# Performance work log

Measured on AMD Instinct MI355X. Metric: run time of the kernel, lower is better.

Reference implementation:

```python
import jax, jax.numpy as jnp
import numpy as np

N_HEADS_ROUTER = 8
N_HEADS_INPUT = 4
LN_EPS = 1e-5

def gelu(x):
    return jax.nn.gelu(x, approximate=False)  # torch F.gelu default (erf)

def mha(x, wq, wk, wv, bq, bk, bv, wo, bo, n_heads):
    # PyTorch nn.MultiheadAttention (batch_first, eval mode)
    B, S, E = x.shape
    d = E // n_heads
    scale = 1.0 / np.sqrt(d).astype(np.float32)
    def split(t):
        return t.reshape(B, S, n_heads, d).transpose(0, 2, 1, 3)  # [B,H,S,d]
    q = split(x @ wq.T + bq)
    k = split(x @ wk.T + bk)
    v = split(x @ wv.T + bv)
    attn = jax.nn.softmax(jnp.einsum('bhqd,bhkd->bhqk', q, k) * scale, axis=-1)
    o = jnp.einsum('bhqk,bhkd->bhqd', attn, v).transpose(0, 2, 1, 3).reshape(B, S, E)
    return o @ wo.T + bo

def layer_norm(x, g, b):
    mu = x.mean(axis=-1, keepdims=True)
    var = ((x - mu) ** 2).mean(axis=-1, keepdims=True)
    return (x - mu) * jax.lax.rsqrt(var + LN_EPS) * g + b

def setup_inputs() -> dict:
    key = jax.random.key(0)
    ks = jax.random.split(key, 20)
    B, S, D, NI, NP = 4, 1024, 1024, 512, 1024
    def rn(k, shape, s=0.02):
        return jax.random.normal(k, shape, jnp.float32) * s
    return {
        'x': jax.random.normal(ks[0], (B, S, D), jnp.float32),
        # DynamicRouter MHA (embed=d_model, 8 heads)
        'r_wq': rn(ks[1], (D, D)), 'r_wk': rn(ks[2], (D, D)), 'r_wv': rn(ks[3], (D, D)),
        'r_bq': jnp.zeros((D,), jnp.float32), 'r_bk': jnp.zeros((D,), jnp.float32), 'r_bv': jnp.zeros((D,), jnp.float32),
        'r_wo': rn(ks[4], (D, D)), 'r_bo': jnp.zeros((D,), jnp.float32),
        'aff_w': rn(ks[5], (NI, D)), 'aff_b': jnp.zeros((NI,), jnp.float32),
        # InputNeurons
        'patterns': rn(ks[6], (NI, D), 0.05),
        'i_wq': rn(ks[7], (NI, NI)), 'i_wk': rn(ks[8], (NI, NI)), 'i_wv': rn(ks[9], (NI, NI)),
        'i_bq': jnp.zeros((NI,), jnp.float32), 'i_bk': jnp.zeros((NI,), jnp.float32), 'i_bv': jnp.zeros((NI,), jnp.float32),
        'i_wo': rn(ks[10], (NI, NI)), 'i_bo': jnp.zeros((NI,), jnp.float32),
        'ln_g': jnp.ones((NI,), jnp.float32), 'ln_b': jnp.zeros((NI,), jnp.float32),
        # ProcessNeurons
        'comb_w': rn(ks[11], (NP, NI), 0.05),
        'proj_w': rn(ks[12], (NP, D), 0.05),
        'k_input': 256,
        'k_process': 512,
    }

def reference(x, r_wq, r_wk, r_wv, r_bq, r_bk, r_bv, r_wo, r_bo, aff_w, aff_b,
              patterns, i_wq, i_wk, i_wv, i_bq, i_bk, i_bv, i_wo, i_bo,
              ln_g, ln_b, comb_w, proj_w, k_input, k_process):
    B, S, D = x.shape
    NI = aff_w.shape[0]
    # --- DynamicRouter ---
    context = mha(x, r_wq, r_wk, r_wv, r_bq, r_bk, r_bv, r_wo, r_bo, N_HEADS_ROUTER)
    affinity = context @ aff_w.T + aff_b           # [B,S,NI]
    scores = affinity.max(axis=1)                  # [B,NI] (max-pool over seq)
    probs = jax.nn.softmax(scores, axis=-1)
    _, idx = jax.lax.top_k(scores, k_input)        # [B,k_in]
    one_hot = jax.nn.one_hot(idx, NI, dtype=probs.dtype).sum(axis=1)  # [B,NI]
    weights = jax.lax.stop_gradient(one_hot - probs) + probs          # straight-through
    # --- InputNeurons ---
    act = gelu(context @ patterns.T)               # [B,S,NI]
    attn_out = mha(act, i_wq, i_wk, i_wv, i_bq, i_bk, i_bv, i_wo, i_bo, N_HEADS_INPUT)
    act = layer_norm(act + attn_out, ln_g, ln_b)
    # --- select input neurons ---
    weighted = act * weights[:, None, :]
    sel = jnp.take_along_axis(weighted, jnp.broadcast_to(idx[:, None, :], (B, S, k_input)), axis=2)  # [B,S,k_in]
    # --- ProcessNeurons ---
    sel_w = comb_w[:, idx].transpose(1, 0, 2)      # [B, NP, k_in]
    pa = gelu(jnp.einsum('bsk,bpk->bsp', sel, sel_w))  # [B,S,NP]
    ps = pa.mean(axis=1)                            # [B,NP]
    _, pidx = jax.lax.top_k(ps, k_process)          # [B,k_p]
    spa = jnp.take_along_axis(pa, jnp.broadcast_to(pidx[:, None, :], (B, S, k_process)), axis=2)  # [B,S,k_p]
    sproj = proj_w[pidx]                            # [B,k_p,D]
    return jnp.einsum('bsk,bkd->bsd', spa, sproj)   # [B,S,D]
```

## Files before the change

### kernel.cpp

```cpp
#include <hip/hip_runtime.h>
#include <math.h>

#define DEVI static __device__ __forceinline__

typedef __attribute__((ext_vector_type(8))) short short8;
typedef __attribute__((ext_vector_type(4))) float f32x4;
typedef unsigned short u16;

DEVI float gelu_f(float x) {
    return 0.5f * x * (1.0f + erff(x * 0.7071067811865475f));
}
DEVI u16 f2bf(float f) {
    unsigned u = __builtin_bit_cast(unsigned, f);
    return (u16)((u + 0x7fffu + ((u >> 16) & 1u)) >> 16);
}
DEVI float bf2f(u16 b) {
    unsigned u = ((unsigned)b) << 16;
    return __builtin_bit_cast(float, u);
}
DEVI void split_bf(float v, u16& h, u16& l) {
    h = f2bf(v);
    l = f2bf(v - bf2f(h));
}

template<int BN, bool SPLIT, bool DO_GELU, int OMODE>
__global__ __launch_bounds__(256, 2)
void gemm_planes(const u16* __restrict__ Agh, const u16* __restrict__ Agl,
                 const u16* __restrict__ Bgh, const u16* __restrict__ Bgl,
                 const float* __restrict__ bias, float* __restrict__ Cf,
                 u16* __restrict__ O1h, u16* __restrict__ O1l,
                 u16* __restrict__ O2h, u16* __restrict__ O2l,
                 u16* __restrict__ O3h, u16* __restrict__ O3l,
                 int M, int N, int K, int HH, int partN)
{
    constexpr int BM = 128, BK = 64, PK = 72;
    constexpr int NPL = SPLIT ? 2 : 1;
    constexpr int MF  = (BN == 128) ? 4 : 2;
    __shared__ __align__(16) u16 As[NPL][BM * PK];
    __shared__ __align__(16) u16 Bs[NPL][BN * PK];
    const int t = threadIdx.x, w = t >> 6, l = t & 63;
    const int lr = l & 15, lg = l >> 4;
    const int m0 = blockIdx.y * BM, n0 = blockIdx.x * BN;
    const int moff = (BN == 128) ? (w >> 1) * 64 : w * 32;
    const int noff = (BN == 128) ? (w & 1) * 64 : 0;
    const int srow = t >> 3, sslot = t & 7;

    f32x4 acc[MF][4];
    #pragma unroll
    for (int i = 0; i < MF; ++i)
        #pragma unroll
        for (int j = 0; j < 4; ++j) acc[i][j] = 0.0f;

    for (int k0 = 0; k0 < K; k0 += BK) {
        __syncthreads();
        #pragma unroll
        for (int p = 0; p < 4; ++p) {
            int row = p * 32 + srow;
            size_t g = (size_t)(m0 + row) * K + k0 + sslot * 8;
            *(uint4*)&As[0][row * PK + sslot * 8] = *(const uint4*)&Agh[g];
            if constexpr (SPLIT)
                *(uint4*)&As[1][row * PK + sslot * 8] = *(const uint4*)&Agl[g];
        }
        #pragma unroll
        for (int p = 0; p < BN / 32; ++p) {
            int row = p * 32 + srow;
            size_t g = (size_t)(n0 + row) * K + k0 + sslot * 8;
            *(uint4*)&Bs[0][row * PK + sslot * 8] = *(const uint4*)&Bgh[g];
            if constexpr (SPLIT)
                *(uint4*)&Bs[1][row * PK + sslot * 8] = *(const uint4*)&Bgl[g];
        }
        __syncthreads();
        #pragma unroll
        for (int ks = 0; ks < 2; ++ks) {
            short8 af[MF][NPL], bfr[4][NPL];
            #pragma unroll
            for (int mf = 0; mf < MF; ++mf) {
                int a = (moff + mf * 16 + lr) * PK + ks * 32 + lg * 8;
                af[mf][0] = *(const short8*)&As[0][a];
                if constexpr (SPLIT) af[mf][1] = *(const short8*)&As[1][a];
            }
            #pragma unroll
            for (int nf = 0; nf < 4; ++nf) {
                int a = (noff + nf * 16 + lr) * PK + ks * 32 + lg * 8;
                bfr[nf][0] = *(const short8*)&Bs[0][a];
                if constexpr (SPLIT) bfr[nf][1] = *(const short8*)&Bs[1][a];
            }
            #pragma unroll
            for (int mf = 0; mf < MF; ++mf)
                #pragma unroll
                for (int nf = 0; nf < 4; ++nf) {
                    acc[mf][nf] = __builtin_amdgcn_mfma_f32_16x16x32_bf16(
                        af[mf][0], bfr[nf][0], acc[mf][nf], 0, 0, 0);
                    if constexpr (SPLIT) {
                        acc[mf][nf] = __builtin_amdgcn_mfma_f32_16x16x32_bf16(
                            af[mf][0], bfr[nf][1], acc[mf][nf], 0, 0, 0);
                        acc[mf][nf] = __builtin_amdgcn_mfma_f32_16x16x32_bf16(
                            af[mf][1], bfr[nf][0], acc[mf][nf], 0, 0, 0);
                    }
                }
        }
    }
    #pragma unroll
    for (int mf = 0; mf < MF; ++mf)
        #pragma unroll
        for (int nf = 0; nf < 4; ++nf) {
            int col  = n0 + noff + nf * 16 + lr;
            int mrow = m0 + moff + mf * 16 + lg * 4;
            float bv = bias ? bias[col] : 0.0f;
            float ov[4];
            #pragma unroll
            for (int r = 0; r < 4; ++r) ov[r] = acc[mf][nf][r] + bv;
            if constexpr (OMODE == 0) {
                #pragma unroll
                for (int r = 0; r < 4; ++r) {
                    float o = ov[r];
                    if constexpr (DO_GELU) o = gelu_f(o);
                    Cf[(size_t)(mrow + r) * N + col] = o;
                }
            } else if constexpr (OMODE == 1) {
                #pragma unroll
                for (int r = 0; r < 4; ++r) {
                    float o = ov[r];
                    if constexpr (DO_GELU) o = gelu_f(o);
                    u16 hb, lb; split_bf(o, hb, lb);
                    O1h[(size_t)(mrow + r) * N + col] = hb;
                    O1l[(size_t)(mrow + r) * N + col] = lb;
                }
            } else if constexpr (OMODE == 3) {
                if (col < partN) {
                    #pragma unroll
                    for (int r = 0; r < 4; ++r) {
                        u16 hb, lb; split_bf(ov[r], hb, lb);
                        O1h[(size_t)(mrow + r) * partN + col] = hb;
                        O1l[(size_t)(mrow + r) * partN + col] = lb;
                    }
                } else if (col < 2 * partN) {
                    int c2 = col - partN;
                    #pragma unroll
                    for (int r = 0; r < 4; ++r) {
                        u16 hb, lb; split_bf(ov[r], hb, lb);
                        O2h[(size_t)(mrow + r) * partN + c2] = hb;
                        O2l[(size_t)(mrow + r) * partN + c2] = lb;
                    }
                } else {
                    int c2 = col - 2 * partN;
                    int hh = c2 >> 7, dd = c2 & 127;
                    int bb = mrow >> 10, s0 = mrow & 1023;
                    size_t idx = ((size_t)(bb * HH + hh) * 128 + dd) * 1024 + s0;
                    ushort4 oh, ol;
                    #pragma unroll
                    for (int r = 0; r < 4; ++r) {
                        u16 hb, lb; split_bf(ov[r], hb, lb);
                        ((u16*)&oh)[r] = hb; ((u16*)&ol)[r] = lb;
                    }
                    *(ushort4*)&O3h[idx] = oh;
                    *(ushort4*)&O3l[idx] = ol;
                }
            } else if constexpr (OMODE == 4) {
                if (col < partN) {
                    #pragma unroll
                    for (int r = 0; r < 4; ++r)
                        Cf[(size_t)(mrow + r) * partN + col] = ov[r];
                } else {
                    int c2 = col - partN;
                    #pragma unroll
                    for (int r = 0; r < 4; ++r) {
                        float o = gelu_f(ov[r]);
                        u16 hb, lb; split_bf(o, hb, lb);
                        O1h[(size_t)(mrow + r) * partN + c2] = hb;
                        O1l[(size_t)(mrow + r) * partN + c2] = lb;
                    }
                }
            }
        }
}

__global__ __launch_bounds__(256, 3)
void attn_planes(const u16* __restrict__ Qh, const u16* __restrict__ Ql,
                 const u16* __restrict__ Kh, const u16* __restrict__ Kl,
                 const u16* __restrict__ Vh, const u16* __restrict__ Vl,
                 u16* __restrict__ Oh, u16* __restrict__ Ol,
                 int S, int Dm, int H, float scale)
{
    __shared__ __align__(16) u16 KsL[2][32 * 136];
    __shared__ __align__(16) u16 VsL[2][128 * 40];
    __shared__ __align__(16) u16 PsL[2][4 * 16 * 40];
    const int t = threadIdx.x, w = t >> 6, l = t & 63;
    const int lr = l & 15, lg = l >> 4;
    const int nqt = gridDim.x;
    const int nwg = nqt * gridDim.y;
    const int fid = blockIdx.y * nqt + blockIdx.x;
    const int nid = (fid & 7) * (nwg >> 3) + (fid >> 3);
    const int bh = nid / nqt, qt = nid - bh * nqt;
    const int b = bh / H, h = bh - b * H;
    const int q0 = qt * 64 + w * 16;
    const size_t qkbase = (size_t)(b * S) * Dm + h * 128;
    const size_t vbase  = (size_t)(b * H + h) * 128 * 1024;

    short8 qhf[4], qlf[4];
    #pragma unroll
    for (int ks = 0; ks < 4; ++ks) {
        size_t g = qkbase + (size_t)(q0 + lr) * Dm + ks * 32 + lg * 8;
        qhf[ks] = *(const short8*)&Qh[g];
        qlf[ks] = *(const short8*)&Ql[g];
    }
    f32x4 accO[8];
    #pragma unroll
    for (int i = 0; i < 8; ++i) accO[i] = 0.0f;
    float ls = 0.0f;
    const int pw = w * 640;

    for (int c0 = 0; c0 < S; c0 += 32) {
        __syncthreads();
        #pragma unroll
        for (int p = 0; p < 2; ++p) {
            int key = p * 16 + (t >> 4);
            int slot = t & 15;
            size_t g = qkbase + (size_t)(c0 + key) * Dm + slot * 8;
            *(uint4*)&KsL[0][key * 136 + slot * 8] = *(const uint4*)&Kh[g];
            *(uint4*)&KsL[1][key * 136 + slot * 8] = *(const uint4*)&Kl[g];
        }
        #pragma unroll
        for (int p = 0; p < 2; ++p) {
            int d = p * 64 + (t >> 2);
            int ksl = t & 3;
            size_t g = vbase + (size_t)d * 1024 + c0 + ksl * 8;
            *(uint4*)&VsL[0][d * 40 + ksl * 8] = *(const uint4*)&Vh[g];
            *(uint4*)&VsL[1][d * 40 + ksl * 8] = *(const uint4*)&Vl[g];
        }
        __syncthreads();
        f32x4 sac[2];
        sac[0] = 0.0f; sac[1] = 0.0f;
        #pragma unroll
        for (int mt = 0; mt < 2; ++mt)
            #pragma unroll
            for (int ks = 0; ks < 4; ++ks) {
                int a = (mt * 16 + lr) * 136 + ks * 32 + lg * 8;
                short8 khf = *(const short8*)&KsL[0][a];
                short8 klf = *(const short8*)&KsL[1][a];
                sac[mt] = __builtin_amdgcn_mfma_f32_16x16x32_bf16(khf, qhf[ks], sac[mt], 0, 0, 0);
                sac[mt] = __builtin_amdgcn_mfma_f32_16x16x32_bf16(khf, qlf[ks], sac[mt], 0, 0, 0);
                sac[mt] = __builtin_amdgcn_mfma_f32_16x16x32_bf16(klf, qhf[ks], sac[mt], 0, 0, 0);
            }
        #pragma unroll
        for (int mt = 0; mt < 2; ++mt)
            #pragma unroll
            for (int rr = 0; rr < 4; ++rr) {
                float p = __expf(sac[mt][rr] * scale);
                ls += p;
                int key = mt * 16 + lg * 4 + rr;
                u16 hb, lb; split_bf(p, hb, lb);
                PsL[0][pw + lr * 40 + key] = hb;
                PsL[1][pw + lr * 40 + key] = lb;
            }
        short8 pah = *(const short8*)&PsL[0][pw + lr * 40 + lg * 8];
        short8 pal = *(const short8*)&PsL[1][pw + lr * 40 + lg * 8];
        #pragma unroll
        for (int nt = 0; nt < 8; ++nt) {
            int a = (nt * 16 + lr) * 40 + lg * 8;
            short8 vhf = *(const short8*)&VsL[0][a];
            short8 vlf = *(const short8*)&VsL[1][a];
            accO[nt] = __builtin_amdgcn_mfma_f32_16x16x32_bf16(pah, vhf, accO[nt], 0, 0, 0);
            accO[nt] = __builtin_amdgcn_mfma_f32_16x16x32_bf16(pah, vlf, accO[nt], 0, 0, 0);
            accO[nt] = __builtin_amdgcn_mfma_f32_16x16x32_bf16(pal, vhf, accO[nt], 0, 0, 0);
        }
    }
    float lt = ls + __shfl_xor(ls, 16, 64);
    lt += __shfl_xor(lt, 32, 64);
    #pragma unroll
    for (int rr = 0; rr < 4; ++rr) {
        float inv = 1.0f / __shfl(lt, lg * 4 + rr, 64);
        size_t rowoff = qkbase + (size_t)(q0 + lg * 4 + rr) * Dm;
        #pragma unroll
        for (int nt = 0; nt < 8; ++nt) {
            float o = accO[nt][rr] * inv;
            u16 hb, lb; split_bf(o, hb, lb);
            Oh[rowoff + nt * 16 + lr] = hb;
            Ol[rowoff + nt * 16 + lr] = lb;
        }
    }
}

__global__ __launch_bounds__(256)
void pack_f32(const float* __restrict__ src, u16* __restrict__ dh,
              u16* __restrict__ dl, int n4)
{
    int i = blockIdx.x * 256 + threadIdx.x;
    if (i >= n4) return;
    float4 v = *(const float4*)&src[i * 4];
    ushort4 hv, lv;
    split_bf(v.x, hv.x, lv.x);
    split_bf(v.y, hv.y, lv.y);
    split_bf(v.z, hv.z, lv.z);
    split_bf(v.w, hv.w, lv.w);
    *(ushort4*)&dh[i * 4] = hv;
    *(ushort4*)&dl[i * 4] = lv;
}

__global__ __launch_bounds__(256)
void packT64(const float* __restrict__ src, u16* __restrict__ dh,
             u16* __restrict__ dl, int R, int C)
{
    __shared__ float tile[64][65];
    int r0 = blockIdx.y * 64, c0 = blockIdx.x * 64;
    int t = threadIdx.x;
    #pragma unroll
    for (int i = 0; i < 16; ++i) {
        int idx = i * 256 + t, rr = idx >> 6, cc = idx & 63;
        tile[rr][cc] = src[(size_t)(r0 + rr) * C + c0 + cc];
    }
    __syncthreads();
    #pragma unroll
    for (int i = 0; i < 16; ++i) {
        int idx = i * 256 + t, rr = idx >> 6, cc = idx & 63;
        float v = tile[cc][rr];
        u16 hb, lb; split_bf(v, hb, lb);
        size_t o = (size_t)(c0 + rr) * R + r0 + cc;
        dh[o] = hb; dl[o] = lb;
    }
}

__global__ __launch_bounds__(256)
void mask_rows(u16* __restrict__ ph, const float* __restrict__ mask)
{
    int i = blockIdx.x * 256 + threadIdx.x;
    int i4 = i * 4;
    int bb = i4 >> 20;
    int col = i4 & 1023;
    ushort4 v = *(ushort4*)&ph[i4];
    float4 m = *(const float4*)&mask[bb * 1024 + col];
    if (m.x == 0.f) v.x = 0;
    if (m.y == 0.f) v.y = 0;
    if (m.z == 0.f) v.z = 0;
    if (m.w == 0.f) v.w = 0;
    *(ushort4*)&ph[i4] = v;
}

__global__ __launch_bounds__(256)
void reduce_max_f32(const float* __restrict__ X, float* __restrict__ P, int S, int N)
{
    int n = blockIdx.x * 256 + threadIdx.x;
    int sc = blockIdx.y, bb = blockIdx.z;
    const float* base = X + ((size_t)bb * S + sc * 64) * N + n;
    float acc = -3.402823466e38f;
    for (int s = 0; s < 64; ++s) acc = fmaxf(acc, base[(size_t)s * N]);
    P[((size_t)bb * 16 + sc) * N + n] = acc;
}

__global__ __launch_bounds__(256)
void reduce_sum_planes(const u16* __restrict__ Xh, const u16* __restrict__ Xl,
                       float* __restrict__ P, int S, int N)
{
    int n = blockIdx.x * 256 + threadIdx.x;
    int sc = blockIdx.y, bb = blockIdx.z;
    size_t base = ((size_t)bb * S + sc * 64) * N + n;
    float acc = 0.f;
    for (int s = 0; s < 64; ++s)
        acc += bf2f(Xh[base + (size_t)s * N]) + bf2f(Xl[base + (size_t)s * N]);
    P[((size_t)bb * 16 + sc) * N + n] = acc;
}

template<int OP>
__global__ __launch_bounds__(256)
void reduce_stage2(const float* __restrict__ P, float* __restrict__ Y, int N, float scl)
{
    int n = blockIdx.x * 256 + threadIdx.x;
    int bb = blockIdx.y;
    float acc = (OP == 0) ? -3.402823466e38f : 0.f;
    for (int s = 0; s < 16; ++s) {
        float v = P[((size_t)bb * 16 + s) * N + n];
        acc = (OP == 0) ? fmaxf(acc, v) : (acc + v);
    }
    Y[(size_t)bb * N + n] = (OP == 0) ? acc : acc * scl;
}

template<int N, int KSEL>
__global__ __launch_bounds__(1024)
void topk_mask_kernel(const float* __restrict__ Sc, float* __restrict__ mask)
{
    __shared__ float v[N];
    __shared__ int   id[N];
    int t = threadIdx.x;
    int b = blockIdx.x;
    v[t]  = Sc[b * N + t];
    id[t] = t;
    __syncthreads();
    for (int k = 2; k <= N; k <<= 1) {
        for (int j = k >> 1; j > 0; j >>= 1) {
            int ixj = t ^ j;
            if (ixj > t) {
                bool dir = ((t & k) == 0);
                float va = v[t], vb = v[ixj];
                int   ia = id[t], ib = id[ixj];
                bool before_b = (vb > va) || (vb == va && ib < ia);
                bool sw = dir ? before_b : !before_b;
                if (sw) { v[t] = vb; v[ixj] = va; id[t] = ib; id[ixj] = ia; }
            }
            __syncthreads();
        }
    }
    mask[b * N + id[t]] = (t < KSEL) ? 1.0f : 0.0f;
}

__global__ __launch_bounds__(256)
void ln_mask_planes(const u16* __restrict__ Xh, const u16* __restrict__ Xl,
                    const u16* __restrict__ Rh, const u16* __restrict__ Rl,
                    const float* __restrict__ gam, const float* __restrict__ bet,
                    const float* __restrict__ mask,
                    u16* __restrict__ Yh, u16* __restrict__ Yl)
{
    int row = blockIdx.x, bb = row >> 10, t = threadIdx.x;
    size_t base = (size_t)row * 512;
    float a1 = bf2f(Xh[base + t]) + bf2f(Xl[base + t])
             + bf2f(Rh[base + t]) + bf2f(Rl[base + t]);
    float a2 = bf2f(Xh[base + t + 256]) + bf2f(Xl[base + t + 256])
             + bf2f(Rh[base + t + 256]) + bf2f(Rl[base + t + 256]);
    float s  = a1 + a2;
    float sq = a1 * a1 + a2 * a2;
    #pragma unroll
    for (int off = 32; off > 0; off >>= 1) {
        s  += __shfl_down(s, off, 64);
        sq += __shfl_down(sq, off, 64);
    }
    __shared__ float red[8];
    int wid = t >> 6, lane = t & 63;
    if (lane == 0) { red[wid] = s; red[wid + 4] = sq; }
    __syncthreads();
    if (t == 0) {
        float st  = red[0] + red[1] + red[2] + red[3];
        float sqt = red[4] + red[5] + red[6] + red[7];
        float mu  = st / 512.0f;
        float var = sqt / 512.0f - mu * mu;
        red[0] = mu;
        red[1] = rsqrtf(var + 1e-5f);
    }
    __syncthreads();
    float mu = red[0], rstd = red[1];
    float y1 = ((a1 - mu) * rstd * gam[t] + bet[t]) * mask[bb * 512 + t];
    float y2 = ((a2 - mu) * rstd * gam[t + 256] + bet[t + 256]) * mask[bb * 512 + t + 256];
    u16 hb, lb;
    split_bf(y1, hb, lb); Yh[base + t] = hb;       Yl[base + t] = lb;
    split_bf(y2, hb, lb); Yh[base + t + 256] = hb; Yl[base + t + 256] = lb;
}

extern "C" void kernel_launch(void* const* d_in, const int* in_sizes, int n_in,
                              void* d_out, int out_size, void* d_ws, size_t ws_size,
                              hipStream_t stream)
{
    (void)in_sizes; (void)n_in; (void)out_size; (void)ws_size;
    const float* x        = (const float*)d_in[0];
    const float* r_wq     = (const float*)d_in[1];
    const float* r_wk     = (const float*)d_in[2];
    const float* r_wv     = (const float*)d_in[3];
    const float* r_bq     = (const float*)d_in[4];
    const float* r_bk     = (const float*)d_in[5];
    const float* r_bv     = (const float*)d_in[6];
    const float* r_wo     = (const float*)d_in[7];
    const float* r_bo     = (const float*)d_in[8];
    const float* aff_w    = (const float*)d_in[9];
    const float* aff_b    = (const float*)d_in[10];
    const float* patterns = (const float*)d_in[11];
    const float* i_wq     = (const float*)d_in[12];
    const float* i_wk     = (const float*)d_in[13];
    const float* i_wv     = (const float*)d_in[14];
    const float* i_bq     = (const float*)d_in[15];
    const float* i_bk     = (const float*)d_in[16];
    const float* i_bv     = (const float*)d_in[17];
    const float* i_wo     = (const float*)d_in[18];
    const float* i_bo     = (const float*)d_in[19];
    const float* ln_g     = (const float*)d_in[20];
    const float* ln_b     = (const float*)d_in[21];
    const float* comb_w   = (const float*)d_in[22];
    const float* proj_w   = (const float*)d_in[23];

    constexpr size_t MBy = 1024 * 1024;
    char* base = (char*)d_ws;

    u16* xh   = (u16*)(base);             u16* xl   = (u16*)(base + 8 * MBy);
    u16* aph  = xh;                        u16* apl  = xl;
    float* aff = (float*)base;
    u16* acth = (u16*)(base + 8 * MBy);   u16* actl = (u16*)(base + 12 * MBy);
    u16* rqh  = (u16*)(base + 16 * MBy);  u16* rql  = (u16*)(base + 24 * MBy);
    u16* ctxh = rqh;                       u16* ctxl = rql;
    u16* pah  = rqh;                       u16* pal  = rql;
    u16* rkh  = (u16*)(base + 32 * MBy);  u16* rkl  = (u16*)(base + 40 * MBy);
    u16* iqh  = (u16*)(base + 32 * MBy);  u16* iql  = (u16*)(base + 36 * MBy);
    u16* ikh  = (u16*)(base + 40 * MBy);  u16* ikl  = (u16*)(base + 44 * MBy);
    u16* a2fh = iqh;                       u16* a2fl = iql;
    u16* lnmh = ikh;                       u16* lnml = ikl;
    u16* rvth = (u16*)(base + 48 * MBy);  u16* rvtl = (u16*)(base + 56 * MBy);
    u16* ivth = (u16*)(base + 48 * MBy);  u16* ivtl = (u16*)(base + 52 * MBy);
    u16* a2ph = (u16*)(base + 56 * MBy);  u16* a2pl = (u16*)(base + 60 * MBy);
    u16* wqkvh = (u16*)(base + 64 * MBy); u16* wqkvl = (u16*)(base + 70 * MBy);
    u16* woh   = (u16*)(base + 64 * MBy); u16* wol   = (u16*)(base + 66 * MBy);
    u16* apbh  = (u16*)(base + 68 * MBy); u16* apbl  = (u16*)(base + 70 * MBy);
    u16* iwqkvh = (u16*)(base + 64 * MBy); u16* iwqkvl = (u16*)(base + 66 * MBy);
    u16* iwoh  = (u16*)(base + 68 * MBy); u16* iwol  = (u16*)(base + 69 * MBy);
    u16* cbh   = (u16*)(base + 70 * MBy); u16* cbl   = (u16*)(base + 71 * MBy);
    u16* pjh   = (u16*)(base + 72 * MBy); u16* pjl   = (u16*)(base + 74 * MBy);
    float* partial = (float*)(base + 76 * MBy);
    float* scores  = (float*)(base + 76 * MBy + 262144);
    float* maskI   = scores + 2048;
    float* ps      = maskI + 2048;
    float* maskP   = ps + 4096;
    float* rbias   = maskP + 4096;
    float* ibias   = rbias + 3072;
    float* apbias  = ibias + 1536;

    const float scale = 0.08838834764831843f;
    dim3 blk(256);

    pack_f32<<<4096, blk, 0, stream>>>(x, xh, xl, 1048576);
    pack_f32<<<1024, blk, 0, stream>>>(r_wq, wqkvh, wqkvl, 262144);
    pack_f32<<<1024, blk, 0, stream>>>(r_wk, wqkvh + 1048576, wqkvl + 1048576, 262144);
    pack_f32<<<1024, blk, 0, stream>>>(r_wv, wqkvh + 2097152, wqkvl + 2097152, 262144);
    hipMemcpyAsync(rbias,        r_bq, 4096, hipMemcpyDeviceToDevice, stream);
    hipMemcpyAsync(rbias + 1024, r_bk, 4096, hipMemcpyDeviceToDevice, stream);
    hipMemcpyAsync(rbias + 2048, r_bv, 4096, hipMemcpyDeviceToDevice, stream);

    gemm_planes<128, true, false, 3><<<dim3(24, 32), blk, 0, stream>>>(
        xh, xl, wqkvh, wqkvl, rbias, nullptr,
        rqh, rql, rkh, rkl, rvth, rvtl, 4096, 3072, 1024, 8, 1024);

    pack_f32<<<1024, blk, 0, stream>>>(r_wo, woh, wol, 262144);
    pack_f32<<<512, blk, 0, stream>>>(aff_w, apbh, apbl, 131072);
    pack_f32<<<512, blk, 0, stream>>>(patterns, apbh + 524288, apbl + 524288, 131072);
    hipMemcpyAsync(apbias, aff_b, 2048, hipMemcpyDeviceToDevice, stream);
    hipMemsetAsync(apbias + 512, 0, 2048, stream);

    attn_planes<<<dim3(16, 32), blk, 0, stream>>>(rqh, rql, rkh, rkl, rvth, rvtl,
                                                  aph, apl, 1024, 1024, 8, scale);
    gemm_planes<128, true, false, 1><<<dim3(8, 32), blk, 0, stream>>>(
        aph, apl, woh, wol, r_bo, nullptr,
        ctxh, ctxl, nullptr, nullptr, nullptr, nullptr, 4096, 1024, 1024, 0, 0);

    gemm_planes<128, true, false, 4><<<dim3(8, 32), blk, 0, stream>>>(
        ctxh, ctxl, apbh, apbl, apbias, aff,
        acth, actl, nullptr, nullptr, nullptr, nullptr, 4096, 1024, 1024, 0, 512);
    reduce_max_f32<<<dim3(2, 16, 4), blk, 0, stream>>>(aff, partial, 1024, 512);
    reduce_stage2<0><<<dim3(2, 4), blk, 0, stream>>>(partial, scores, 512, 1.0f);
    topk_mask_kernel<512, 256><<<dim3(4), dim3(512), 0, stream>>>(scores, maskI);

    pack_f32<<<256, blk, 0, stream>>>(i_wq, iwqkvh, iwqkvl, 65536);
    pack_f32<<<256, blk, 0, stream>>>(i_wk, iwqkvh + 262144, iwqkvl + 262144, 65536);
    pack_f32<<<256, blk, 0, stream>>>(i_wv, iwqkvh + 524288, iwqkvl + 524288, 65536);
    pack_f32<<<256, blk, 0, stream>>>(i_wo, iwoh, iwol, 65536);
    pack_f32<<<512, blk, 0, stream>>>(comb_w, cbh, cbl, 131072);
    packT64<<<dim3(16, 16), blk, 0, stream>>>(proj_w, pjh, pjl, 1024, 1024);
    hipMemcpyAsync(ibias,        i_bq, 2048, hipMemcpyDeviceToDevice, stream);
    hipMemcpyAsync(ibias + 512,  i_bk, 2048, hipMemcpyDeviceToDevice, stream);
    hipMemcpyAsync(ibias + 1024, i_bv, 2048, hipMemcpyDeviceToDevice, stream);

    gemm_planes<128, true, false, 3><<<dim3(12, 32), blk, 0, stream>>>(
        acth, actl, iwqkvh, iwqkvl, ibias, nullptr,
        iqh, iql, ikh, ikl, ivth, ivtl, 4096, 1536, 512, 4, 512);
    attn_planes<<<dim3(16, 16), blk, 0, stream>>>(iqh, iql, ikh, ikl, ivth, ivtl,
                                                  a2ph, a2pl, 1024, 512, 4, scale);
    gemm_planes<64, true, false, 1><<<dim3(8, 32), blk, 0, stream>>>(
        a2ph, a2pl, iwoh, iwol, i_bo, nullptr,
        a2fh, a2fl, nullptr, nullptr, nullptr, nullptr, 4096, 512, 512, 0, 0);
    ln_mask_planes<<<dim3(4096), blk, 0, stream>>>(acth, actl, a2fh, a2fl,
                                                   ln_g, ln_b, maskI, lnmh, lnml);

    gemm_planes<128, true, true, 1><<<dim3(8, 32), blk, 0, stream>>>(
        lnmh, lnml, cbh, cbl, nullptr, nullptr,
        pah, pal, nullptr, nullptr, nullptr, nullptr, 4096, 1024, 512, 0, 0);
    reduce_sum_planes<<<dim3(4, 16, 4), blk, 0, stream>>>(pah, pal, partial, 1024, 1024);
    reduce_stage2<1><<<dim3(4, 4), blk, 0, stream>>>(partial, ps, 1024, 1.0f / 1024.0f);
    topk_mask_kernel<1024, 512><<<dim3(4), dim3(1024), 0, stream>>>(ps, maskP);
    mask_rows<<<4096, blk, 0, stream>>>(pah, maskP);

    gemm_planes<128, false, false, 0><<<dim3(8, 32), blk, 0, stream>>>(
        pah, nullptr, pjh, nullptr, nullptr, (float*)d_out,
        nullptr, nullptr, nullptr, nullptr, nullptr, nullptr, 4096, 1024, 1024, 0, 0);
}
```

Measured before the change: 546.0 us.

## Prefetch GEMM tiles to registers, fuse column reductions into epilogues, batch packing

```diff
diff --git a/kernel.cpp b/kernel.cpp
--- a/kernel.cpp
+++ b/kernel.cpp
@@ -36,6 +36,7 @@
     constexpr int BM = 128, BK = 64, PK = 72;
     constexpr int NPL = SPLIT ? 2 : 1;
     constexpr int MF  = (BN == 128) ? 4 : 2;
+    constexpr int NB  = BN / 32;
     __shared__ __align__(16) u16 As[NPL][BM * PK];
     __shared__ __align__(16) u16 Bs[NPL][BN * PK];
     const int t = threadIdx.x, w = t >> 6, l = t & 63;
@@ -51,25 +52,41 @@
         #pragma unroll
         for (int j = 0; j < 4; ++j) acc[i][j] = 0.0f;
 
-    for (int k0 = 0; k0 < K; k0 += BK) {
-        __syncthreads();
+    uint4 ar[4][NPL], br[NB][NPL];
+    auto LOADR = [&](int k0) {
         #pragma unroll
         for (int p = 0; p < 4; ++p) {
             int row = p * 32 + srow;
             size_t g = (size_t)(m0 + row) * K + k0 + sslot * 8;
-            *(uint4*)&As[0][row * PK + sslot * 8] = *(const uint4*)&Agh[g];
-            if constexpr (SPLIT)
-                *(uint4*)&As[1][row * PK + sslot * 8] = *(const uint4*)&Agl[g];
-        }
-        #pragma unroll
-        for (int p = 0; p < BN / 32; ++p) {
+            ar[p][0] = *(const uint4*)&Agh[g];
+            if constexpr (SPLIT) ar[p][1] = *(const uint4*)&Agl[g];
+        }
+        #pragma unroll
+        for (int p = 0; p < NB; ++p) {
             int row = p * 32 + srow;
             size_t g = (size_t)(n0 + row) * K + k0 + sslot * 8;
-            *(uint4*)&Bs[0][row * PK + sslot * 8] = *(const uint4*)&Bgh[g];
-            if constexpr (SPLIT)
-                *(uint4*)&Bs[1][row * PK + sslot * 8] = *(const uint4*)&Bgl[g];
-        }
+            br[p][0] = *(const uint4*)&Bgh[g];
+            if constexpr (SPLIT) br[p][1] = *(const uint4*)&Bgl[g];
+        }
+    };
+
+    LOADR(0);
+    for (int k0 = 0; k0 < K; k0 += BK) {
         __syncthreads();
+        #pragma unroll
+        for (int p = 0; p < 4; ++p) {
+            int row = p * 32 + srow;
+            *(uint4*)&As[0][row * PK + sslot * 8] = ar[p][0];
+            if constexpr (SPLIT) *(uint4*)&As[1][row * PK + sslot * 8] = ar[p][1];
+        }
+        #pragma unroll
+        for (int p = 0; p < NB; ++p) {
+            int row = p * 32 + srow;
+            *(uint4*)&Bs[0][row * PK + sslot * 8] = br[p][0];
+            if constexpr (SPLIT) *(uint4*)&Bs[1][row * PK + sslot * 8] = br[p][1];
+        }
+        __syncthreads();
+        if (k0 + BK < K) LOADR(k0 + BK);
         #pragma unroll
         for (int ks = 0; ks < 2; ++ks) {
             short8 af[MF][NPL], bfr[4][NPL];
@@ -99,6 +116,13 @@
                     }
                 }
         }
+    }
+
+    float colred[4];
+    if constexpr (OMODE == 4) {
+        colred[0] = colred[1] = colred[2] = colred[3] = -3.402823466e38f;
+    } else if constexpr (OMODE == 5) {
+        colred[0] = colred[1] = colred[2] = colred[3] = 0.0f;
     }
     #pragma unroll
     for (int mf = 0; mf < MF; ++mf)
@@ -157,10 +181,10 @@
                     *(ushort4*)&O3l[idx] = ol;
                 }
             } else if constexpr (OMODE == 4) {
-                if (col < partN) {
+                if (n0 < partN) {
                     #pragma unroll
                     for (int r = 0; r < 4; ++r)
-                        Cf[(size_t)(mrow + r) * partN + col] = ov[r];
+                        colred[nf] = fmaxf(colred[nf], ov[r]);
                 } else {
                     int c2 = col - partN;
                     #pragma unroll
@@ -171,8 +195,40 @@
                         O1l[(size_t)(mrow + r) * partN + c2] = lb;
                     }
                 }
+            } else if constexpr (OMODE == 5) {
+                #pragma unroll
+                for (int r = 0; r < 4; ++r) {
+                    float o = gelu_f(ov[r]);
+                    colred[nf] += o;
+                    u16 hb, lb; split_bf(o, hb, lb);
+                    O1h[(size_t)(mrow + r) * N + col] = hb;
+                    O1l[(size_t)(mrow + r) * N + col] = lb;
+                }
             }
         }
+    if constexpr (OMODE == 4 || OMODE == 5) {
+        bool doRed = (OMODE == 5) || (n0 < partN);
+        if (doRed) {
+            __syncthreads();
+            float* sred = (float*)&As[0][0];
+            #pragma unroll
+            for (int nf = 0; nf < 4; ++nf) sred[t * 4 + nf] = colred[nf];
+            __syncthreads();
+            if (t < 128) {
+                int cl = t, lrr = cl & 15, nff = (cl & 63) >> 4, wb = cl >> 6;
+                float a = (OMODE == 4) ? -3.402823466e38f : 0.0f;
+                #pragma unroll
+                for (int k2 = 0; k2 < 2; ++k2)
+                    #pragma unroll
+                    for (int l2 = 0; l2 < 4; ++l2) {
+                        float v = sred[(((wb + 2 * k2) * 64) + l2 * 16 + lrr) * 4 + nff];
+                        if constexpr (OMODE == 4) a = fmaxf(a, v); else a += v;
+                    }
+                int stride = (OMODE == 4) ? partN : N;
+                Cf[(size_t)blockIdx.y * stride + n0 + cl] = a;
+            }
+        }
+    }
 }
 
 __global__ __launch_bounds__(256, 3)
@@ -281,6 +337,25 @@
     }
 }
 
+struct PSeg { const float* s; u16* h; u16* l; int n4; int pad; };
+struct PArgs { PSeg g[8]; };
+
+__global__ __launch_bounds__(256)
+void pack_many(PArgs a)
+{
+    PSeg sg = a.g[blockIdx.y];
+    int i = blockIdx.x * 256 + threadIdx.x;
+    if (i >= sg.n4) return;
+    float4 v = *(const float4*)&sg.s[i * 4];
+    ushort4 hv, lv;
+    split_bf(v.x, hv.x, lv.x);
+    split_bf(v.y, hv.y, lv.y);
+    split_bf(v.z, hv.z, lv.z);
+    split_bf(v.w, hv.w, lv.w);
+    *(ushort4*)&sg.h[i * 4] = hv;
+    *(ushort4*)&sg.l[i * 4] = lv;
+}
+
 __global__ __launch_bounds__(256)
 void pack_f32(const float* __restrict__ src, u16* __restrict__ dh,
               u16* __restrict__ dl, int n4)
@@ -317,6 +392,23 @@
         u16 hb, lb; split_bf(v, hb, lb);
         size_t o = (size_t)(c0 + rr) * R + r0 + cc;
         dh[o] = hb; dl[o] = lb;
+    }
+}
+
+__global__ __launch_bounds__(1024)
+void concat_bias(const float* rq, const float* rk, const float* rv,
+                 const float* iq, const float* ik, const float* iv,
+                 const float* ab, float* rb, float* ib, float* apb)
+{
+    int t = threadIdx.x;
+    rb[t]        = rq[t];
+    rb[1024 + t] = rk[t];
+    rb[2048 + t] = rv[t];
+    apb[t] = (t < 512) ? ab[t] : 0.0f;
+    if (t < 512) {
+        ib[t]        = iq[t];
+        ib[512 + t]  = ik[t];
+        ib[1024 + t] = iv[t];
     }
 }
 
@@ -336,42 +428,19 @@
     *(ushort4*)&ph[i4] = v;
 }
 
-__global__ __launch_bounds__(256)
-void reduce_max_f32(const float* __restrict__ X, float* __restrict__ P, int S, int N)
-{
-    int n = blockIdx.x * 256 + threadIdx.x;
-    int sc = blockIdx.y, bb = blockIdx.z;
-    const float* base = X + ((size_t)bb * S + sc * 64) * N + n;
-    float acc = -3.402823466e38f;
-    for (int s = 0; s < 64; ++s) acc = fmaxf(acc, base[(size_t)s * N]);
-    P[((size_t)bb * 16 + sc) * N + n] = acc;
-}
-
-__global__ __launch_bounds__(256)
-void reduce_sum_planes(const u16* __restrict__ Xh, const u16* __restrict__ Xl,
-                       float* __restrict__ P, int S, int N)
-{
-    int n = blockIdx.x * 256 + threadIdx.x;
-    int sc = blockIdx.y, bb = blockIdx.z;
-    size_t base = ((size_t)bb * S + sc * 64) * N + n;
-    float acc = 0.f;
-    for (int s = 0; s < 64; ++s)
-        acc += bf2f(Xh[base + (size_t)s * N]) + bf2f(Xl[base + (size_t)s * N]);
-    P[((size_t)bb * 16 + sc) * N + n] = acc;
-}
-
 template<int OP>
 __global__ __launch_bounds__(256)
-void reduce_stage2(const float* __restrict__ P, float* __restrict__ Y, int N, float scl)
+void reduce8(const float* __restrict__ P, float* __restrict__ Y, int N, float scl)
 {
     int n = blockIdx.x * 256 + threadIdx.x;
-    int bb = blockIdx.y;
-    float acc = (OP == 0) ? -3.402823466e38f : 0.f;
-    for (int s = 0; s < 16; ++s) {
-        float v = P[((size_t)bb * 16 + s) * N + n];
-        acc = (OP == 0) ? fmaxf(acc, v) : (acc + v);
-    }
-    Y[(size_t)bb * N + n] = (OP == 0) ? acc : acc * scl;
+    int b = blockIdx.y;
+    float a = (OP == 0) ? -3.402823466e38f : 0.0f;
+    #pragma unroll
+    for (int r = 0; r < 8; ++r) {
+        float v = P[(size_t)(b * 8 + r) * N + n];
+        if (OP == 0) a = fmaxf(a, v); else a += v;
+    }
+    Y[(size_t)b * N + n] = (OP == 0) ? a : a * scl;
 }
 
 template<int N, int KSEL>
@@ -478,7 +547,8 @@
 
     u16* xh   = (u16*)(base);             u16* xl   = (u16*)(base + 8 * MBy);
     u16* aph  = xh;                        u16* apl  = xl;
-    float* aff = (float*)base;
+    u16* cbh  = (u16*)(base);             u16* cbl  = (u16*)(base + 1 * MBy);
+    u16* pjh  = (u16*)(base + 2 * MBy);   u16* pjl  = (u16*)(base + 4 * MBy);
     u16* acth = (u16*)(base + 8 * MBy);   u16* actl = (u16*)(base + 12 * MBy);
     u16* rqh  = (u16*)(base + 16 * MBy);  u16* rql  = (u16*)(base + 24 * MBy);
     u16* ctxh = rqh;                       u16* ctxl = rql;
@@ -491,13 +561,13 @@
     u16* rvth = (u16*)(base + 48 * MBy);  u16* rvtl = (u16*)(base + 56 * MBy);
     u16* ivth = (u16*)(base + 48 * MBy);  u16* ivtl = (u16*)(base + 52 * MBy);
     u16* a2ph = (u16*)(base + 56 * MBy);  u16* a2pl = (u16*)(base + 60 * MBy);
-    u16* wqkvh = (u16*)(base + 64 * MBy); u16* wqkvl = (u16*)(base + 70 * MBy);
-    u16* woh   = (u16*)(base + 64 * MBy); u16* wol   = (u16*)(base + 66 * MBy);
-    u16* apbh  = (u16*)(base + 68 * MBy); u16* apbl  = (u16*)(base + 70 * MBy);
-    u16* iwqkvh = (u16*)(base + 64 * MBy); u16* iwqkvl = (u16*)(base + 66 * MBy);
-    u16* iwoh  = (u16*)(base + 68 * MBy); u16* iwol  = (u16*)(base + 69 * MBy);
-    u16* cbh   = (u16*)(base + 70 * MBy); u16* cbl   = (u16*)(base + 71 * MBy);
-    u16* pjh   = (u16*)(base + 72 * MBy); u16* pjl   = (u16*)(base + 74 * MBy);
+    u16* wqkvh  = (u16*)(base + 64 * MBy); u16* wqkvl = (u16*)(base + 70 * MBy);
+    u16* woh    = (u16*)(base + 64 * MBy); u16* wol   = (u16*)(base + 66 * MBy);
+    u16* apbh   = (u16*)(base + 68 * MBy); u16* apbl  = (u16*)(base + 70 * MBy);
+    u16* iwqkvh = (u16*)(base + 72 * MBy);
+    u16* iwqkvl = (u16*)(base + 72 * MBy + 1572864);
+    u16* iwoh   = (u16*)(base + 75 * MBy);
+    u16* iwol   = (u16*)(base + 75 * MBy + 524288);
     float* partial = (float*)(base + 76 * MBy);
     float* scores  = (float*)(base + 76 * MBy + 262144);
     float* maskI   = scores + 2048;
@@ -510,23 +580,32 @@
     const float scale = 0.08838834764831843f;
     dim3 blk(256);
 
-    pack_f32<<<4096, blk, 0, stream>>>(x, xh, xl, 1048576);
-    pack_f32<<<1024, blk, 0, stream>>>(r_wq, wqkvh, wqkvl, 262144);
-    pack_f32<<<1024, blk, 0, stream>>>(r_wk, wqkvh + 1048576, wqkvl + 1048576, 262144);
-    pack_f32<<<1024, blk, 0, stream>>>(r_wv, wqkvh + 2097152, wqkvl + 2097152, 262144);
-    hipMemcpyAsync(rbias,        r_bq, 4096, hipMemcpyDeviceToDevice, stream);
-    hipMemcpyAsync(rbias + 1024, r_bk, 4096, hipMemcpyDeviceToDevice, stream);
-    hipMemcpyAsync(rbias + 2048, r_bv, 4096, hipMemcpyDeviceToDevice, stream);
+    concat_bias<<<dim3(1), dim3(1024), 0, stream>>>(r_bq, r_bk, r_bv,
+        i_bq, i_bk, i_bv, aff_b, rbias, ibias, apbias);
+    {
+        PArgs a{};
+        a.g[0] = {x,    xh,              xl,              1048576, 0};
+        a.g[1] = {r_wq, wqkvh,           wqkvl,           262144,  0};
+        a.g[2] = {r_wk, wqkvh + 1048576, wqkvl + 1048576, 262144,  0};
+        a.g[3] = {r_wv, wqkvh + 2097152, wqkvl + 2097152, 262144,  0};
+        pack_many<<<dim3(4096, 4), blk, 0, stream>>>(a);
+    }
 
     gemm_planes<128, true, false, 3><<<dim3(24, 32), blk, 0, stream>>>(
         xh, xl, wqkvh, wqkvl, rbias, nullptr,
         rqh, rql, rkh, rkl, rvth, rvtl, 4096, 3072, 1024, 8, 1024);
 
-    pack_f32<<<1024, blk, 0, stream>>>(r_wo, woh, wol, 262144);
-    pack_f32<<<512, blk, 0, stream>>>(aff_w, apbh, apbl, 131072);
-    pack_f32<<<512, blk, 0, stream>>>(patterns, apbh + 524288, apbl + 524288, 131072);
-    hipMemcpyAsync(apbias, aff_b, 2048, hipMemcpyDeviceToDevice, stream);
-    hipMemsetAsync(apbias + 512, 0, 2048, stream);
+    {
+        PArgs a{};
+        a.g[0] = {r_wo,     woh,             wol,             262144, 0};
+        a.g[1] = {aff_w,    apbh,            apbl,            131072, 0};
+        a.g[2] = {patterns, apbh + 524288,   apbl + 524288,   131072, 0};
+        a.g[3] = {i_wq,     iwqkvh,          iwqkvl,          65536,  0};
+        a.g[4] = {i_wk,     iwqkvh + 262144, iwqkvl + 262144, 65536,  0};
+        a.g[5] = {i_wv,     iwqkvh + 524288, iwqkvl + 524288, 65536,  0};
+        a.g[6] = {i_wo,     iwoh,            iwol,            65536,  0};
+        pack_many<<<dim3(1024, 7), blk, 0, stream>>>(a);
+    }
 
     attn_planes<<<dim3(16, 32), blk, 0, stream>>>(rqh, rql, rkh, rkl, rvth, rvtl,
                                                   aph, apl, 1024, 1024, 8, scale);
@@ -535,21 +614,13 @@
         ctxh, ctxl, nullptr, nullptr, nullptr, nullptr, 4096, 1024, 1024, 0, 0);
 
     gemm_planes<128, true, false, 4><<<dim3(8, 32), blk, 0, stream>>>(
-        ctxh, ctxl, apbh, apbl, apbias, aff,
+        ctxh, ctxl, apbh, apbl, apbias, partial,
         acth, actl, nullptr, nullptr, nullptr, nullptr, 4096, 1024, 1024, 0, 512);
-    reduce_max_f32<<<dim3(2, 16, 4), blk, 0, stream>>>(aff, partial, 1024, 512);
-    reduce_stage2<0><<<dim3(2, 4), blk, 0, stream>>>(partial, scores, 512, 1.0f);
+    reduce8<0><<<dim3(2, 4), blk, 0, stream>>>(partial, scores, 512, 1.0f);
     topk_mask_kernel<512, 256><<<dim3(4), dim3(512), 0, stream>>>(scores, maskI);
 
-    pack_f32<<<256, blk, 0, stream>>>(i_wq, iwqkvh, iwqkvl, 65536);
-    pack_f32<<<256, blk, 0, stream>>>(i_wk, iwqkvh + 262144, iwqkvl + 262144, 65536);
-    pack_f32<<<256, blk, 0, stream>>>(i_wv, iwqkvh + 524288, iwqkvl + 524288, 65536);
-    pack_f32<<<256, blk, 0, stream>>>(i_wo, iwoh, iwol, 65536);
     pack_f32<<<512, blk, 0, stream>>>(comb_w, cbh, cbl, 131072);
     packT64<<<dim3(16, 16), blk, 0, stream>>>(proj_w, pjh, pjl, 1024, 1024);
-    hipMemcpyAsync(ibias,        i_bq, 2048, hipMemcpyDeviceToDevice, stream);
-    hipMemcpyAsync(ibias + 512,  i_bk, 2048, hipMemcpyDeviceToDevice, stream);
-    hipMemcpyAsync(ibias + 1024, i_bv, 2048, hipMemcpyDeviceToDevice, stream);
 
     gemm_planes<128, true, false, 3><<<dim3(12, 32), blk, 0, stream>>>(
         acth, actl, iwqkvh, iwqkvl, ibias, nullptr,
@@ -562,11 +633,10 @@
     ln_mask_planes<<<dim3(4096), blk, 0, stream>>>(acth, actl, a2fh, a2fl,
                                                    ln_g, ln_b, maskI, lnmh, lnml);
 
-    gemm_planes<128, true, true, 1><<<dim3(8, 32), blk, 0, stream>>>(
-        lnmh, lnml, cbh, cbl, nullptr, nullptr,
+    gemm_planes<128, true, true, 5><<<dim3(8, 32), blk, 0, stream>>>(
+        lnmh, lnml, cbh, cbl, nullptr, partial,
         pah, pal, nullptr, nullptr, nullptr, nullptr, 4096, 1024, 512, 0, 0);
-    reduce_sum_planes<<<dim3(4, 16, 4), blk, 0, stream>>>(pah, pal, partial, 1024, 1024);
-    reduce_stage2<1><<<dim3(4, 4), blk, 0, stream>>>(partial, ps, 1024, 1.0f / 1024.0f);
+    reduce8<1><<<dim3(4, 4), blk, 0, stream>>>(partial, ps, 1024, 1.0f / 1024.0f);
     topk_mask_kernel<1024, 512><<<dim3(4), dim3(1024), 0, stream>>>(ps, maskP);
     mask_rows<<<4096, blk, 0, stream>>>(pah, maskP);
 
```

After: 889.5 us. 62.9% more time.
